# Kernel tuning notes

Measured on AMD Instinct MI355X. Metric: run time of the kernel, lower is better.

Reference implementation:

```python
import jax, jax.numpy as jnp
import numpy as np

B, L, D, H = 2, 2048, 1024, 16
DH = D // H            # head depth = 64
LEN_CONTEXT = 2048 + 1 # module stores len_context + 1


def setup_inputs() -> dict:
    key = jax.random.key(0)
    ks = jax.random.split(key, 9)
    s = 0.02
    return {
        "query": jax.random.normal(ks[0], (B, L, D), jnp.float32),
        "key":   jax.random.normal(ks[1], (B, L, D), jnp.float32),
        "value": jax.random.normal(ks[2], (B, L, D), jnp.float32),
        "Wq": jax.random.normal(ks[3], (D, D), jnp.float32) * s,
        "bq": jnp.zeros((D,), jnp.float32),
        "Wk": jax.random.normal(ks[4], (D, D), jnp.float32) * s,
        "bk": jnp.zeros((D,), jnp.float32),
        "Wv": jax.random.normal(ks[5], (D, D), jnp.float32) * s,
        "bv": jnp.zeros((D,), jnp.float32),
        "Wo": jax.random.normal(ks[6], (D, D), jnp.float32) * s,
        "bo": jnp.zeros((D,), jnp.float32),
        "rel": jax.random.normal(ks[7], (LEN_CONTEXT, DH), jnp.float32) * s,
    }


def _split_heads(x):
    # [B, L, D] -> [B, H, L, DH]
    return x.reshape(B, L, H, DH).transpose(0, 2, 1, 3)


def reference(query, key, value, Wq, bq, Wk, bk, Wv, bv, Wo, bo, rel):
    q = _split_heads(query @ Wq + bq)   # [B,H,L,DH]
    k = _split_heads(key @ Wk + bk)
    v = _split_heads(value @ Wv + bv)

    # relative embedding slice: rel[max(0, len_context - len_q):]
    start = max(0, LEN_CONTEXT - L)
    e = rel[start:, :]                  # [M, DH], M = L here
    M = e.shape[0]

    qe = jnp.einsum('bhld,md->bhlm', q, e)  # [B,H,L,M]

    # _qe_masking: keep qe[l, m] where m >= M-1-l (upper anti-triangle)
    mask = (jnp.arange(M)[None, :] >= (M - 1 - jnp.arange(L))[:, None]).astype(qe.dtype)
    qe = qe * mask

    # _skewing: pad 1 on left of last dim, reshape swapping last two dims, drop first row
    padded = jnp.pad(qe, ((0, 0), (0, 0), (0, 0), (1, 0)))        # [B,H,L,M+1]
    reshaped = padded.reshape(B, H, M + 1, L)
    srel = reshaped[:, :, 1:, :]                                  # [B,H,L,L] (len_k == len_q)

    logits = (jnp.einsum('bhld,bhmd->bhlm', q, k) + srel) / jnp.sqrt(jnp.float32(DH))
    # NOTE: the original code builds a directional mask but never adds it to logits
    attn = jax.nn.softmax(logits, axis=-1)
    out = jnp.einsum('bhlm,bhmd->bhld', attn, v)                  # [B,H,L,DH]
    out = out.transpose(0, 2, 1, 3).reshape(B, L, D)
    return out @ Wo + bo
```

## Files before the change

kernel.cpp:

```cpp
#include <hip/hip_runtime.h>
#include <hip/hip_bf16.h>


typedef __bf16 v8bf __attribute__((ext_vector_type(8)));
typedef __bf16 v4bf __attribute__((ext_vector_type(4)));
typedef float f32x4 __attribute__((ext_vector_type(4)));
typedef float f32x16 __attribute__((ext_vector_type(16)));

#define MFMA16(A,B,C) __builtin_amdgcn_mfma_f32_16x16x32_bf16((A),(B),(C),0,0,0)
#define MFMA32(A,B,C) __builtin_amdgcn_mfma_f32_32x32x16_bf16((A),(B),(C),0,0,0)

constexpr float kQScale = 0.1803368801111244f;

__global__ __launch_bounds__(256)
void cast_rel(const float* __restrict__ rel, __bf16* __restrict__ E)
{
    const int i = blockIdx.x * 256 + threadIdx.x;
    if (i >= 2304 * 16) return;
    const int base = i * 4;
    const int row = base >> 6;
    const int prow = row - 128;
    v4bf o;
    if (prow >= 0 && prow < 2048) {
        const float4 v = *reinterpret_cast<const float4*>(&rel[(size_t)(prow + 1) * 64 + (base & 63)]);
        o[0] = (__bf16)v.x; o[1] = (__bf16)v.y; o[2] = (__bf16)v.z; o[3] = (__bf16)v.w;
    } else {
        o[0] = (__bf16)0.f; o[1] = (__bf16)0.f; o[2] = (__bf16)0.f; o[3] = (__bf16)0.f;
    }
    *reinterpret_cast<v4bf*>(&E[base]) = o;
}

__global__ __launch_bounds__(256)
void transpose_cast_w4(const float* __restrict__ W0, const float* __restrict__ W1,
                       const float* __restrict__ W2, const float* __restrict__ W3,
                       __bf16* __restrict__ Wt4)
{
    __shared__ float tile[64][65];
    const int z = blockIdx.z;
    const float* W = (z == 0) ? W0 : (z == 1) ? W1 : (z == 2) ? W2 : W3;
    __bf16* Wt = Wt4 + (size_t)z * 1048576;
    const int r0 = blockIdx.y * 64, c0 = blockIdx.x * 64;
    const int tr = threadIdx.x >> 4;
    const int tc = (threadIdx.x & 15) * 4;
    #pragma unroll
    for (int p = 0; p < 4; ++p) {
        const int r = tr + p * 16;
        const float4 v = *reinterpret_cast<const float4*>(&W[(size_t)(r0 + r) * 1024 + c0 + tc]);
        tile[r][tc + 0] = v.x; tile[r][tc + 1] = v.y; tile[r][tc + 2] = v.z; tile[r][tc + 3] = v.w;
    }
    __syncthreads();
    #pragma unroll
    for (int p = 0; p < 4; ++p) {
        const int cr = tr + p * 16;
        v4bf o;
        o[0] = (__bf16)tile[tc + 0][cr];
        o[1] = (__bf16)tile[tc + 1][cr];
        o[2] = (__bf16)tile[tc + 2][cr];
        o[3] = (__bf16)tile[tc + 3][cr];
        *reinterpret_cast<v4bf*>(&Wt[(size_t)(c0 + cr) * 1024 + r0 + tc]) = o;
    }
}

template <bool ABF16>
__device__ __forceinline__
void gemm_body(const float* __restrict__ Af, const __bf16* __restrict__ Ab,
               const __bf16* __restrict__ Wt, const float* __restrict__ bias,
               float* __restrict__ Cf, __bf16* __restrict__ Cb, int mode,
               float oscale, int bx, int by)
{
    __shared__ __bf16 As[2][128 * 64];
    __shared__ __bf16 Ws[2][128 * 64];
    const int tid = threadIdx.x;
    const int wid = tid >> 6, lane = tid & 63, g = lane >> 4, li = lane & 15;
    const int r0 = by * 128, c0 = bx * 128;
    const int wr = wid >> 1, wc = wid & 1;
    const int sr = tid >> 3, sb = tid & 7;

    f32x4 acc[4][4];
    #pragma unroll
    for (int a = 0; a < 4; ++a)
        #pragma unroll
        for (int b2 = 0; b2 < 4; ++b2) acc[a][b2] = f32x4{0.f, 0.f, 0.f, 0.f};

    v8bf areg[4], wreg[4];

    auto loadA = [&](int p, int kt) -> v8bf {
        if constexpr (ABF16) {
            return *reinterpret_cast<const v8bf*>(&Ab[(size_t)(r0 + sr + 32 * p) * 1024 + kt + sb * 8]);
        } else {
            const float* ar = &Af[(size_t)(r0 + sr + 32 * p) * 1024 + kt + sb * 8];
            const float4 f0 = *reinterpret_cast<const float4*>(ar);
            const float4 f1 = *reinterpret_cast<const float4*>(ar + 4);
            v8bf a8;
            a8[0] = (__bf16)f0.x; a8[1] = (__bf16)f0.y; a8[2] = (__bf16)f0.z; a8[3] = (__bf16)f0.w;
            a8[4] = (__bf16)f1.x; a8[5] = (__bf16)f1.y; a8[6] = (__bf16)f1.z; a8[7] = (__bf16)f1.w;
            return a8;
        }
    };
    auto loadW = [&](int p, int kt) -> v8bf {
        return *reinterpret_cast<const v8bf*>(&Wt[(size_t)(c0 + sr + 32 * p) * 1024 + kt + sb * 8]);
    };

    #pragma unroll
    for (int p = 0; p < 4; ++p) { areg[p] = loadA(p, 0); wreg[p] = loadW(p, 0); }
    #pragma unroll
    for (int p = 0; p < 4; ++p) {
        const int row = sr + 32 * p;
        *reinterpret_cast<v8bf*>(&As[0][row * 64 + ((sb ^ (row & 7)) << 3)]) = areg[p];
        *reinterpret_cast<v8bf*>(&Ws[0][row * 64 + ((sb ^ (row & 7)) << 3)]) = wreg[p];
    }
    __syncthreads();

    for (int ki = 0; ki < 16; ++ki) {
        const int cur = ki & 1;
        if (ki < 15) {
            const int kt = (ki + 1) * 64;
            #pragma unroll
            for (int p = 0; p < 4; ++p) { areg[p] = loadA(p, kt); wreg[p] = loadW(p, kt); }
        }
        #pragma unroll
        for (int ks = 0; ks < 2; ++ks) {
            v8bf af[4], bfr[4];
            #pragma unroll
            for (int fm = 0; fm < 4; ++fm) {
                const int row = wr * 64 + fm * 16 + li;
                af[fm] = *reinterpret_cast<const v8bf*>(
                    &As[cur][row * 64 + (((ks * 4 + g) ^ (row & 7)) << 3)]);
            }
            #pragma unroll
            for (int fn = 0; fn < 4; ++fn) {
                const int row = wc * 64 + fn * 16 + li;
                bfr[fn] = *reinterpret_cast<const v8bf*>(
                    &Ws[cur][row * 64 + (((ks * 4 + g) ^ (row & 7)) << 3)]);
            }
            __builtin_amdgcn_s_setprio(1);
            #pragma unroll
            for (int fm = 0; fm < 4; ++fm)
                #pragma unroll
                for (int fn = 0; fn < 4; ++fn)
                    acc[fm][fn] = MFMA16(af[fm], bfr[fn], acc[fm][fn]);
            __builtin_amdgcn_s_setprio(0);
        }
        if (ki < 15) {
            const int nxt = cur ^ 1;
            #pragma unroll
            for (int p = 0; p < 4; ++p) {
                const int row = sr + 32 * p;
                *reinterpret_cast<v8bf*>(&As[nxt][row * 64 + ((sb ^ (row & 7)) << 3)]) = areg[p];
                *reinterpret_cast<v8bf*>(&Ws[nxt][row * 64 + ((sb ^ (row & 7)) << 3)]) = wreg[p];
            }
        }
        __syncthreads();
    }

    #pragma unroll
    for (int fn = 0; fn < 4; ++fn) {
        const int col = c0 + wc * 64 + fn * 16 + li;
        const float bb = bias[col];
        #pragma unroll
        for (int fm = 0; fm < 4; ++fm) {
            if (mode == 2) {
                const int row = r0 + wr * 64 + fm * 16 + 4 * g;
                const int b = row >> 11, l = row & 2047;
                const int h = col >> 6, dh = col & 63;
                v4bf pk;
                #pragma unroll
                for (int reg = 0; reg < 4; ++reg)
                    pk[reg] = (__bf16)(acc[fm][fn][reg] + bb);
                *reinterpret_cast<v4bf*>(&Cb[((size_t)((b * 16 + h) * 64 + dh)) * 2048 + l]) = pk;
            } else {
                #pragma unroll
                for (int reg = 0; reg < 4; ++reg) {
                    const int row = r0 + wr * 64 + fm * 16 + 4 * g + reg;
                    const float val = acc[fm][fn][reg] + bb;
                    if (mode == 0) {
                        Cf[(size_t)row * 1024 + col] = val;
                    } else {
                        const int b = row >> 11, l = row & 2047, h = col >> 6, dh = col & 63;
                        Cb[((size_t)(b * 16 + h) * 2048 + l) * 64 + dh] = (__bf16)(val * oscale);
                    }
                }
            }
        }
    }
}

__device__ __forceinline__ void xcd_remap_gemm(int& bx, int& by)
{
    const int flat = by * 8 + bx;
    const int xcd = flat & 7;
    const int idx = flat >> 3;
    by = xcd * 4 + (idx & 3);
    bx = idx >> 2;
}

__global__ __launch_bounds__(256)
void gemm_proj3(const float* __restrict__ Aq, const float* __restrict__ Ak,
                const float* __restrict__ Av, const __bf16* __restrict__ Wt4,
                const float* __restrict__ bq, const float* __restrict__ bk,
                const float* __restrict__ bv, __bf16* __restrict__ qo,
                __bf16* __restrict__ ko, __bf16* __restrict__ vto)
{
    const int z = blockIdx.z;
    const float* A = (z == 0) ? Aq : (z == 1) ? Ak : Av;
    const __bf16* Wt = Wt4 + (size_t)z * 1048576;
    const float* bias = (z == 0) ? bq : (z == 1) ? bk : bv;
    __bf16* Cb = (z == 0) ? qo : (z == 1) ? ko : vto;
    const float osc = (z == 0) ? kQScale : 1.0f;
    int bx = blockIdx.x, by = blockIdx.y;
    xcd_remap_gemm(bx, by);
    gemm_body<false>(A, nullptr, Wt, bias, nullptr, Cb, (z == 2) ? 2 : 1, osc, bx, by);
}

__global__ __launch_bounds__(256)
void gemm_out(const __bf16* __restrict__ A, const __bf16* __restrict__ Wt,
              const float* __restrict__ bias, float* __restrict__ C)
{
    int bx = blockIdx.x, by = blockIdx.y;
    xcd_remap_gemm(bx, by);
    gemm_body<true>(nullptr, A, Wt, bias, C, nullptr, 0, 1.0f, bx, by);
}

__global__ __launch_bounds__(256, 2)
void attn_mfma(const __bf16* __restrict__ q, const __bf16* __restrict__ k,
               const __bf16* __restrict__ vt, const __bf16* __restrict__ Ep,
               __bf16* __restrict__ ao)
{
    __shared__ __bf16 Kl[2][64 * 64];
    __shared__ __bf16 Vl[2][64 * 64];
    __shared__ __bf16 Tl[4][32 * 128];
    __shared__ __bf16 Pl[4][32 * 64];

    const int tid = threadIdx.x;
    const int wid = tid >> 6;
    const int lane = tid & 63;
    const int l31 = lane & 31;
    const int g2 = lane >> 5;
    const int xsh = (l31 & 7) << 3;

    const int flat = blockIdx.y * 16 + blockIdx.x;
    const int jj_ = flat >> 3;
    const int bh = (flat & 7) * 4 + (jj_ >> 4);
    const int qt = jj_ & 15;

    const int l0 = qt * 128;
    const int lw0 = l0 + wid * 32;
    const size_t hbase = (size_t)bh * (2048 * 64);
    const __bf16* qp = q + hbase;
    const __bf16* kp = k + hbase;
    const __bf16* vtp = vt + hbase;
    const int wb0 = 1984 - l0 - 32 * wid;

    __bf16* Tw = &Tl[wid][0];
    __bf16* Pw = &Pl[wid][0];

    v8bf qf[4];
    {
        const __bf16* qrow = qp + (size_t)(lw0 + l31) * 64 + g2 * 8;
        qf[0] = *reinterpret_cast<const v8bf*>(qrow);
        qf[1] = *reinterpret_cast<const v8bf*>(qrow + 16);
        qf[2] = *reinterpret_cast<const v8bf*>(qrow + 32);
        qf[3] = *reinterpret_cast<const v8bf*>(qrow + 48);
    }

    const int sr = tid >> 3, sb = tid & 7;

    auto eload = [&](int baseRow, v8bf eb[8]) {
        #pragma unroll
        for (int jc = 0; jc < 2; ++jc)
            #pragma unroll
            for (int ks = 0; ks < 4; ++ks)
                eb[jc * 4 + ks] = *reinterpret_cast<const v8bf*>(
                    Ep + (long)(baseRow + jc * 32 + l31) * 64 + ks * 16 + g2 * 8);
    };

    auto tgemm = [&](const v8bf eb[8], int colBase) {
        #pragma unroll
        for (int jc = 0; jc < 2; ++jc) {
            f32x16 tacc;
            #pragma unroll
            for (int r = 0; r < 16; ++r) tacc[r] = 0.f;
            __builtin_amdgcn_s_setprio(1);
            #pragma unroll
            for (int ks = 0; ks < 4; ++ks)
                tacc = MFMA32(eb[jc * 4 + ks], qf[ks], tacc);
            __builtin_amdgcn_s_setprio(0);
            #pragma unroll
            for (int r2 = 0; r2 < 4; ++r2) {
                v4bf w;
                w[0] = (__bf16)tacc[4 * r2 + 0]; w[1] = (__bf16)tacc[4 * r2 + 1];
                w[2] = (__bf16)tacc[4 * r2 + 2]; w[3] = (__bf16)tacc[4 * r2 + 3];
                const int col = colBase + jc * 32 + 8 * r2 + 4 * g2;
                *reinterpret_cast<v4bf*>(Tw + l31 * 128 + (col ^ xsh)) = w;
            }
        }
    };

    {
        const v8bf k0a = *reinterpret_cast<const v8bf*>(kp + (size_t)sr * 64 + sb * 8);
        const v8bf k0b = *reinterpret_cast<const v8bf*>(kp + (size_t)(sr + 32) * 64 + sb * 8);
        const v8bf v0a = *reinterpret_cast<const v8bf*>(vtp + (size_t)sr * 2048 + sb * 8);
        const v8bf v0b = *reinterpret_cast<const v8bf*>(vtp + (size_t)(sr + 32) * 2048 + sb * 8);
        v8bf ebA[8], ebB[8];
        eload(wb0, ebA);
        eload(wb0 + 64, ebB);
        *reinterpret_cast<v8bf*>(&Kl[0][sr * 64 + ((sb ^ (sr & 7)) << 3)]) = k0a;
        *reinterpret_cast<v8bf*>(&Kl[0][(sr + 32) * 64 + ((sb ^ (sr & 7)) << 3)]) = k0b;
        *reinterpret_cast<v8bf*>(&Vl[0][sr * 64 + ((sb ^ (sr & 7)) << 3)]) = v0a;
        *reinterpret_cast<v8bf*>(&Vl[0][(sr + 32) * 64 + ((sb ^ (sr & 7)) << 3)]) = v0b;
        __syncthreads();
        tgemm(ebA, 0);
        tgemm(ebB, 64);
    }

    f32x16 oacc[2];
    #pragma unroll
    for (int dc = 0; dc < 2; ++dc)
        #pragma unroll
        for (int r = 0; r < 16; ++r) oacc[dc][r] = 0.f;
    float lrow = 0.f;

    for (int t = 0; t < 32; ++t) {
        const int m0 = t * 64;
        const int cur = t & 1, nxt = cur ^ 1;
        const bool lastT = (t == 31);
        const bool needRel = (m0 <= lw0 + 31);
        const bool fullAdd = (m0 + 63 <= lw0);
        const bool needTnext = (m0 + 64 <= lw0 + 31);
        const int lob = 64 * (t & 1);

        v8bf ebN[8];
        if (needTnext) eload(wb0 + 64 * t + 128, ebN);

        v8bf kra, krb, vra, vrb;
        if (!lastT) {
            const int m1 = m0 + 64;
            kra = *reinterpret_cast<const v8bf*>(kp + (size_t)(m1 + sr) * 64 + sb * 8);
            krb = *reinterpret_cast<const v8bf*>(kp + (size_t)(m1 + sr + 32) * 64 + sb * 8);
            vra = *reinterpret_cast<const v8bf*>(vtp + (size_t)sr * 2048 + m1 + sb * 8);
            vrb = *reinterpret_cast<const v8bf*>(vtp + (size_t)(sr + 32) * 2048 + m1 + sb * 8);
        }

        #pragma unroll
        for (int mc = 0; mc < 2; ++mc) {
            f32x16 sacc;
            #pragma unroll
            for (int r = 0; r < 16; ++r) sacc[r] = 0.f;
            __builtin_amdgcn_s_setprio(1);
            #pragma unroll
            for (int ks = 0; ks < 4; ++ks) {
                const int row = mc * 32 + l31;
                const v8bf kb = *reinterpret_cast<const v8bf*>(
                    &Kl[cur][row * 64 + (((2 * ks + g2) ^ (l31 & 7)) << 3)]);
                sacc = MFMA32(kb, qf[ks], sacc);
            }
            __builtin_amdgcn_s_setprio(0);

            if (needRel) {
                const int cb = 63 - l31 + lob;
                if (fullAdd) {
                    #pragma unroll
                    for (int r2 = 0; r2 < 4; ++r2)
                        #pragma unroll
                        for (int i2 = 0; i2 < 4; ++i2) {
                            const int mtl = mc * 32 + 8 * r2 + 4 * g2 + i2;
                            const int c = (cb + mtl) & 127;
                            sacc[4 * r2 + i2] += (float)Tw[l31 * 128 + (c ^ xsh)];
                        }
                } else {
                    const int R = lw0 + l31 - m0;
                    #pragma unroll
                    for (int r2 = 0; r2 < 4; ++r2)
                        #pragma unroll
                        for (int i2 = 0; i2 < 4; ++i2) {
                            const int mtl = mc * 32 + 8 * r2 + 4 * g2 + i2;
                            const int c = (cb + mtl) & 127;
                            const float tv = (float)Tw[l31 * 128 + (c ^ xsh)];
                            sacc[4 * r2 + i2] += (mtl <= R) ? tv : 0.f;
                        }
                }
            }

            #pragma unroll
            for (int jj = 0; jj < 4; ++jj) {
                const float p0 = exp2f(sacc[4 * jj + 0]);
                const float p1 = exp2f(sacc[4 * jj + 1]);
                const float p2 = exp2f(sacc[4 * jj + 2]);
                const float p3 = exp2f(sacc[4 * jj + 3]);
                lrow += (p0 + p1) + (p2 + p3);
                v4bf w;
                w[0] = (__bf16)p0; w[1] = (__bf16)p1; w[2] = (__bf16)p2; w[3] = (__bf16)p3;
                const int col = mc * 32 + 8 * jj + 4 * g2;
                *reinterpret_cast<v4bf*>(Pw + l31 * 64 + (col ^ xsh)) = w;
            }
        }

        if (needTnext) tgemm(ebN, lob);

        #pragma unroll
        for (int ks = 0; ks < 4; ++ks) {
            const v8bf pa = *reinterpret_cast<const v8bf*>(
                Pw + l31 * 64 + ((ks * 16 + g2 * 8) ^ xsh));
            __builtin_amdgcn_s_setprio(1);
            #pragma unroll
            for (int dc = 0; dc < 2; ++dc) {
                const int row = dc * 32 + l31;
                const v8bf vb = *reinterpret_cast<const v8bf*>(
                    &Vl[cur][row * 64 + (((2 * ks + g2) ^ (l31 & 7)) << 3)]);
                oacc[dc] = MFMA32(vb, pa, oacc[dc]);
            }
            __builtin_amdgcn_s_setprio(0);
        }

        if (!lastT) {
            *reinterpret_cast<v8bf*>(&Kl[nxt][sr * 64 + ((sb ^ (sr & 7)) << 3)]) = kra;
            *reinterpret_cast<v8bf*>(&Kl[nxt][(sr + 32) * 64 + ((sb ^ (sr & 7)) << 3)]) = krb;
            *reinterpret_cast<v8bf*>(&Vl[nxt][sr * 64 + ((sb ^ (sr & 7)) << 3)]) = vra;
            *reinterpret_cast<v8bf*>(&Vl[nxt][(sr + 32) * 64 + ((sb ^ (sr & 7)) << 3)]) = vrb;
        }
        __syncthreads();
    }

    lrow += __shfl_xor(lrow, 32);
    const float inv = 1.0f / lrow;

    __syncthreads();
    __bf16* Ol = &Tl[0][0];
    #pragma unroll
    for (int dc = 0; dc < 2; ++dc)
        #pragma unroll
        for (int r2 = 0; r2 < 4; ++r2) {
            v4bf w;
            w[0] = (__bf16)(oacc[dc][4 * r2 + 0] * inv);
            w[1] = (__bf16)(oacc[dc][4 * r2 + 1] * inv);
            w[2] = (__bf16)(oacc[dc][4 * r2 + 2] * inv);
            w[3] = (__bf16)(oacc[dc][4 * r2 + 3] * inv);
            const int d0 = dc * 32 + 8 * r2 + 4 * g2;
            *reinterpret_cast<v4bf*>(Ol + (wid * 32 + l31) * 72 + d0) = w;
        }
    __syncthreads();

    const int b = bh >> 4, h = bh & 15;
    #pragma unroll
    for (int p = 0; p < 4; ++p) {
        const int row = p * 32 + (tid >> 3);
        const v8bf w = *reinterpret_cast<const v8bf*>(Ol + row * 72 + (tid & 7) * 8);
        *reinterpret_cast<v8bf*>(ao + (size_t)(b * 2048 + l0 + row) * 1024 + h * 64 + (tid & 7) * 8) = w;
    }
}

extern "C" void kernel_launch(void* const* d_in, const int* in_sizes, int n_in,
                              void* d_out, int out_size, void* d_ws, size_t ws_size,
                              hipStream_t stream) {
    (void)in_sizes; (void)n_in; (void)out_size; (void)ws_size;
    const float* query = (const float*)d_in[0];
    const float* key   = (const float*)d_in[1];
    const float* value = (const float*)d_in[2];
    const float* Wq    = (const float*)d_in[3];
    const float* bq    = (const float*)d_in[4];
    const float* Wk    = (const float*)d_in[5];
    const float* bk    = (const float*)d_in[6];
    const float* Wv    = (const float*)d_in[7];
    const float* bv    = (const float*)d_in[8];
    const float* Wo    = (const float*)d_in[9];
    const float* bo    = (const float*)d_in[10];
    const float* rel   = (const float*)d_in[11];
    float* out = (float*)d_out;

    __bf16* q_bf  = (__bf16*)d_ws;
    __bf16* k_bf  = q_bf + 4194304;
    __bf16* vt_bf = k_bf + 4194304;
    __bf16* Wt4   = vt_bf + 4194304;
    __bf16* E_pad = Wt4 + 4194304;
    __bf16* aob   = E_pad + 147456;

    const dim3 blk(256);

    cast_rel<<<144, blk, 0, stream>>>(rel, E_pad);
    transpose_cast_w4<<<dim3(16, 16, 4), blk, 0, stream>>>(Wq, Wk, Wv, Wo, Wt4);
    gemm_proj3<<<dim3(8, 32, 3), blk, 0, stream>>>(query, key, value, Wt4,
                                                   bq, bk, bv, q_bf, k_bf, vt_bf);
    attn_mfma<<<dim3(16, 32), blk, 0, stream>>>(q_bf, k_bf, vt_bf,
                                                E_pad + 128 * 64, aob);
    gemm_out<<<dim3(8, 32), blk, 0, stream>>>(aob, Wt4 + 3 * 1048576, bo, out);
}
```

Baseline: 187.2 us.

## Stage GEMM bf16 tiles via global_load_lds and fuse rel cast into weight prep

The bf16 operand tiles of the projection and output GEMMs are now copied straight from global memory into LDS with global_load_lds instead of passing through registers. Each lane's source column is XOR-swizzled so the existing LDS swizzled read pattern still holds. The fp32 activation path still loads, converts and stores through registers. Separately, the rel-embedding cast kernel is merged into the weight transpose kernel as an extra grid slice, which saves one kernel launch.

```diff
diff --git a/kernel.cpp b/kernel.cpp
--- a/kernel.cpp
+++ b/kernel.cpp
@@ -12,31 +12,38 @@
 
 constexpr float kQScale = 0.1803368801111244f;
 
+__device__ __forceinline__ void gload_lds16(const void* g, void* l)
+{
+    __builtin_amdgcn_global_load_lds(
+        (const __attribute__((address_space(1))) void*)g,
+        (__attribute__((address_space(3))) void*)l, 16, 0, 0);
+}
+
 __global__ __launch_bounds__(256)
-void cast_rel(const float* __restrict__ rel, __bf16* __restrict__ E)
-{
-    const int i = blockIdx.x * 256 + threadIdx.x;
-    if (i >= 2304 * 16) return;
-    const int base = i * 4;
-    const int row = base >> 6;
-    const int prow = row - 128;
-    v4bf o;
-    if (prow >= 0 && prow < 2048) {
-        const float4 v = *reinterpret_cast<const float4*>(&rel[(size_t)(prow + 1) * 64 + (base & 63)]);
-        o[0] = (__bf16)v.x; o[1] = (__bf16)v.y; o[2] = (__bf16)v.z; o[3] = (__bf16)v.w;
-    } else {
-        o[0] = (__bf16)0.f; o[1] = (__bf16)0.f; o[2] = (__bf16)0.f; o[3] = (__bf16)0.f;
-    }
-    *reinterpret_cast<v4bf*>(&E[base]) = o;
-}
-
-__global__ __launch_bounds__(256)
-void transpose_cast_w4(const float* __restrict__ W0, const float* __restrict__ W1,
-                       const float* __restrict__ W2, const float* __restrict__ W3,
-                       __bf16* __restrict__ Wt4)
-{
+void prep_wr(const float* __restrict__ W0, const float* __restrict__ W1,
+             const float* __restrict__ W2, const float* __restrict__ W3,
+             const float* __restrict__ rel, __bf16* __restrict__ Wt4,
+             __bf16* __restrict__ E)
+{
+    const int z = blockIdx.z;
+    if (z == 4) {
+        const int i = (blockIdx.y * 16 + blockIdx.x) * 256 + threadIdx.x;
+        if (i >= 2304 * 16) return;
+        const int base = i * 4;
+        const int row = base >> 6;
+        const int prow = row - 128;
+        v4bf o;
+        if (prow >= 0 && prow < 2048) {
+            const float4 v = *reinterpret_cast<const float4*>(&rel[(size_t)(prow + 1) * 64 + (base & 63)]);
+            o[0] = (__bf16)v.x; o[1] = (__bf16)v.y; o[2] = (__bf16)v.z; o[3] = (__bf16)v.w;
+        } else {
+            o[0] = (__bf16)0.f; o[1] = (__bf16)0.f; o[2] = (__bf16)0.f; o[3] = (__bf16)0.f;
+        }
+        *reinterpret_cast<v4bf*>(&E[base]) = o;
+        return;
+    }
+
     __shared__ float tile[64][65];
-    const int z = blockIdx.z;
     const float* W = (z == 0) ? W0 : (z == 1) ? W1 : (z == 2) ? W2 : W3;
     __bf16* Wt = Wt4 + (size_t)z * 1048576;
     const int r0 = blockIdx.y * 64, c0 = blockIdx.x * 64;
@@ -82,32 +89,48 @@
         #pragma unroll
         for (int b2 = 0; b2 < 4; ++b2) acc[a][b2] = f32x4{0.f, 0.f, 0.f, 0.f};
 
-    v8bf areg[4], wreg[4];
-
-    auto loadA = [&](int p, int kt) -> v8bf {
-        if constexpr (ABF16) {
-            return *reinterpret_cast<const v8bf*>(&Ab[(size_t)(r0 + sr + 32 * p) * 1024 + kt + sb * 8]);
-        } else {
-            const float* ar = &Af[(size_t)(r0 + sr + 32 * p) * 1024 + kt + sb * 8];
-            const float4 f0 = *reinterpret_cast<const float4*>(ar);
-            const float4 f1 = *reinterpret_cast<const float4*>(ar + 4);
-            v8bf a8;
-            a8[0] = (__bf16)f0.x; a8[1] = (__bf16)f0.y; a8[2] = (__bf16)f0.z; a8[3] = (__bf16)f0.w;
-            a8[4] = (__bf16)f1.x; a8[5] = (__bf16)f1.y; a8[6] = (__bf16)f1.z; a8[7] = (__bf16)f1.w;
-            return a8;
+    const int dmaRow = lane >> 3;
+    const int dmaCol = ((lane & 7) ^ (dmaRow & 7)) * 8;
+
+    auto dmaW = [&](int buf, int kt) {
+        #pragma unroll
+        for (int c = 0; c < 4; ++c) {
+            const int rb = wid * 32 + c * 8;
+            gload_lds16(&Wt[(size_t)(c0 + rb + dmaRow) * 1024 + kt + dmaCol],
+                        &Ws[buf][rb * 64]);
         }
     };
-    auto loadW = [&](int p, int kt) -> v8bf {
-        return *reinterpret_cast<const v8bf*>(&Wt[(size_t)(c0 + sr + 32 * p) * 1024 + kt + sb * 8]);
+    auto dmaA = [&](int buf, int kt) {
+        #pragma unroll
+        for (int c = 0; c < 4; ++c) {
+            const int rb = wid * 32 + c * 8;
+            gload_lds16(&Ab[(size_t)(r0 + rb + dmaRow) * 1024 + kt + dmaCol],
+                        &As[buf][rb * 64]);
+        }
     };
-
-    #pragma unroll
-    for (int p = 0; p < 4; ++p) { areg[p] = loadA(p, 0); wreg[p] = loadW(p, 0); }
-    #pragma unroll
-    for (int p = 0; p < 4; ++p) {
-        const int row = sr + 32 * p;
-        *reinterpret_cast<v8bf*>(&As[0][row * 64 + ((sb ^ (row & 7)) << 3)]) = areg[p];
-        *reinterpret_cast<v8bf*>(&Ws[0][row * 64 + ((sb ^ (row & 7)) << 3)]) = wreg[p];
+    auto loadAf = [&](int p, int kt) -> v8bf {
+        const float* ar = &Af[(size_t)(r0 + sr + 32 * p) * 1024 + kt + sb * 8];
+        const float4 f0 = *reinterpret_cast<const float4*>(ar);
+        const float4 f1 = *reinterpret_cast<const float4*>(ar + 4);
+        v8bf a8;
+        a8[0] = (__bf16)f0.x; a8[1] = (__bf16)f0.y; a8[2] = (__bf16)f0.z; a8[3] = (__bf16)f0.w;
+        a8[4] = (__bf16)f1.x; a8[5] = (__bf16)f1.y; a8[6] = (__bf16)f1.z; a8[7] = (__bf16)f1.w;
+        return a8;
+    };
+
+    v8bf areg[4];
+
+    dmaW(0, 0);
+    if constexpr (ABF16) {
+        dmaA(0, 0);
+    } else {
+        #pragma unroll
+        for (int p = 0; p < 4; ++p) areg[p] = loadAf(p, 0);
+        #pragma unroll
+        for (int p = 0; p < 4; ++p) {
+            const int row = sr + 32 * p;
+            *reinterpret_cast<v8bf*>(&As[0][row * 64 + ((sb ^ (row & 7)) << 3)]) = areg[p];
+        }
     }
     __syncthreads();
 
@@ -115,8 +138,13 @@
         const int cur = ki & 1;
         if (ki < 15) {
             const int kt = (ki + 1) * 64;
-            #pragma unroll
-            for (int p = 0; p < 4; ++p) { areg[p] = loadA(p, kt); wreg[p] = loadW(p, kt); }
+            dmaW(cur ^ 1, kt);
+            if constexpr (ABF16) {
+                dmaA(cur ^ 1, kt);
+            } else {
+                #pragma unroll
+                for (int p = 0; p < 4; ++p) areg[p] = loadAf(p, kt);
+            }
         }
         #pragma unroll
         for (int ks = 0; ks < 2; ++ks) {
@@ -142,12 +170,13 @@
             __builtin_amdgcn_s_setprio(0);
         }
         if (ki < 15) {
-            const int nxt = cur ^ 1;
-            #pragma unroll
-            for (int p = 0; p < 4; ++p) {
-                const int row = sr + 32 * p;
-                *reinterpret_cast<v8bf*>(&As[nxt][row * 64 + ((sb ^ (row & 7)) << 3)]) = areg[p];
-                *reinterpret_cast<v8bf*>(&Ws[nxt][row * 64 + ((sb ^ (row & 7)) << 3)]) = wreg[p];
+            if constexpr (!ABF16) {
+                const int nxt = cur ^ 1;
+                #pragma unroll
+                for (int p = 0; p < 4; ++p) {
+                    const int row = sr + 32 * p;
+                    *reinterpret_cast<v8bf*>(&As[nxt][row * 64 + ((sb ^ (row & 7)) << 3)]) = areg[p];
+                }
             }
         }
         __syncthreads();
@@ -476,8 +505,7 @@
 
     const dim3 blk(256);
 
-    cast_rel<<<144, blk, 0, stream>>>(rel, E_pad);
-    transpose_cast_w4<<<dim3(16, 16, 4), blk, 0, stream>>>(Wq, Wk, Wv, Wo, Wt4);
+    prep_wr<<<dim3(16, 16, 5), blk, 0, stream>>>(Wq, Wk, Wv, Wo, rel, Wt4, E_pad);
     gemm_proj3<<<dim3(8, 32, 3), blk, 0, stream>>>(query, key, value, Wt4,
                                                    bq, bk, bv, q_bf, k_bf, vt_bf);
     attn_mfma<<<dim3(16, 32), blk, 0, stream>>>(q_bf, k_bf, vt_bf,
```

Measured after the change: 189.8 us. About the same (+1.4%).
